# Kernel tuning notes

Measured on AMD Instinct MI355X. Metric: run time of the kernel, lower is better.

The kernel has to match this reference:

```python
import jax, jax.numpy as jnp
import numpy as np


def setup_inputs() -> dict:
    key = jax.random.key(0)
    k1, k2, k3 = jax.random.split(key, 3)
    S, B, H, D = 1024, 32, 512, 1024  # max_len, batch, bin_rnn_size, bin_rep_size
    hidden = jax.random.normal(k1, (2, B, H), dtype=jnp.float32)
    encoder_outputs = jax.random.normal(k2, (S, B, D), dtype=jnp.float32)
    # nn.Linear(D, D) params; scale W for numerically sane softmax logits
    W = jax.random.normal(k3, (D, D), dtype=jnp.float32) / np.float32(np.sqrt(D))
    b = jnp.zeros((D,), dtype=jnp.float32)
    return {"hidden": hidden, "encoder_outputs": encoder_outputs, "W": W, "b": b}


def reference(hidden, encoder_outputs, W, b):
    # method == 'general'
    B = hidden.shape[1]
    # torch.reshape((-1, B, 2H)).squeeze() == C-order flatten -> [B, 2H]
    h = hidden.reshape(B, -1)                                   # [B, D]
    energy = jnp.einsum('sbd,ed->sbe', encoder_outputs, W) + b  # Linear: x @ W.T + b
    # batch_product_luong + sum over features == contraction
    attn_energies = jnp.einsum('bd,sbd->bs', h, energy)         # [B, S]
    alpha = jax.nn.softmax(attn_energies, axis=1)[:, None, :]   # [B, 1, S]
    # alpha.bmm(encoder_outputs.transpose(0,1)) -> [B, 1, D]
    reps = jnp.einsum('bos,sbd->bod', alpha, encoder_outputs)
    return (reps, alpha)
```

## Files before the change

kernel.cpp:

```cpp
#include <hip/hip_runtime.h>

#define S 1024
#define B 32
#define D 1024
#define NCH 32
#define CH (S / NCH)
#define RPW (CH / 4)
#define NPAIR (RPW / 2)
#define ECH 8
#define EC 128

#define PG_OFF   0
#define LOG_OFF  (PG_OFF + ECH * B * D)
#define MARR_OFF (LOG_OFF + B * S)
#define LARR_OFF (MARR_OFF + NCH * B)
#define PACC_OFF (LARR_OFF + NCH * B)

__global__ __launch_bounds__(256) void kG(const float* __restrict__ hid,
                                          const float* __restrict__ W,
                                          float* __restrict__ ws) {
    const int d  = blockIdx.x * 256 + threadIdx.x;
    const int b  = blockIdx.y;
    const int e0 = blockIdx.z * EC;
    const float* __restrict__ hrow = hid + b * D;
    float acc = 0.f;
    #pragma unroll 8
    for (int e = e0; e < e0 + EC; ++e)
        acc = fmaf(hrow[e], W[(size_t)e * D + d], acc);
    ws[PG_OFF + ((size_t)blockIdx.z * B + b) * D + d] = acc;
}

__global__ __launch_bounds__(256) void kB(const float* __restrict__ enc,
                                          float* __restrict__ ws) {
    const int tid  = threadIdx.x;
    const int lane = tid & 63;
    const int wid  = tid >> 6;
    const int c    = blockIdx.x;
    const int b    = blockIdx.y;

    float* pg     = ws + PG_OFF;
    float* logits = ws + LOG_OFF;
    float* marr   = ws + MARR_OFF;
    float* larr   = ws + LARR_OFF;
    float* pacc   = ws + PACC_OFF;

    __shared__ float4 g_sh[256];
    __shared__ float4 sacc[4 * 256];
    __shared__ float sm[4], sl[4];

    const float4* encb = (const float4*)enc;
    const int row0 = c * CH + wid * RPW;
    const size_t rstride = (size_t)B * (D / 4);
    size_t base = ((size_t)row0 * B + b) * (D / 4) + lane;

    float4 cur[8], nxt[8];
    #pragma unroll
    for (int j = 0; j < 4; ++j) {
        cur[j]     = encb[base + j * 64];
        cur[4 + j] = encb[base + rstride + j * 64];
    }
    #pragma unroll
    for (int j = 0; j < 4; ++j) {
        nxt[j]     = encb[base + 2 * rstride + j * 64];
        nxt[4 + j] = encb[base + 3 * rstride + j * 64];
    }

    {
        float4 s4 = {0.f, 0.f, 0.f, 0.f};
        #pragma unroll
        for (int ec = 0; ec < ECH; ++ec) {
            float4 v = ((const float4*)(pg + (size_t)(ec * B + b) * D))[tid];
            s4.x += v.x; s4.y += v.y; s4.z += v.z; s4.w += v.w;
        }
        g_sh[tid] = s4;
    }
    __syncthreads();
    float4 gv[4];
    #pragma unroll
    for (int j = 0; j < 4; ++j) gv[j] = g_sh[j * 64 + lane];

    float m = -3.0e38f, l = 0.f;
    float4 acc[4] = {{0,0,0,0},{0,0,0,0},{0,0,0,0},{0,0,0,0}};

    #pragma unroll
    for (int p = 0; p < NPAIR; ++p) {
        float pd0 = 0.f, pd1 = 0.f;
        #pragma unroll
        for (int j = 0; j < 4; ++j) {
            pd0 += cur[j].x * gv[j].x + cur[j].y * gv[j].y +
                   cur[j].z * gv[j].z + cur[j].w * gv[j].w;
            pd1 += cur[4+j].x * gv[j].x + cur[4+j].y * gv[j].y +
                   cur[4+j].z * gv[j].z + cur[4+j].w * gv[j].w;
        }
        #pragma unroll
        for (int off = 1; off < 64; off <<= 1) {
            pd0 += __shfl_xor(pd0, off, 64);
            pd1 += __shfl_xor(pd1, off, 64);
        }
        if (lane == 0) {
            logits[b * S + row0 + 2 * p]     = pd0;
            logits[b * S + row0 + 2 * p + 1] = pd1;
        }
        float mn  = fmaxf(m, pd0);
        float sc0 = __expf(m - mn);
        float pA  = __expf(pd0 - mn);
        float mn2 = fmaxf(mn, pd1);
        float sc1 = __expf(mn - mn2);
        float pB  = __expf(pd1 - mn2);
        float s01 = sc0 * sc1;
        float a0  = pA * sc1;
        l = l * s01 + a0 + pB;
        #pragma unroll
        for (int j = 0; j < 4; ++j) {
            acc[j].x = acc[j].x * s01 + a0 * cur[j].x + pB * cur[4+j].x;
            acc[j].y = acc[j].y * s01 + a0 * cur[j].y + pB * cur[4+j].y;
            acc[j].z = acc[j].z * s01 + a0 * cur[j].z + pB * cur[4+j].z;
            acc[j].w = acc[j].w * s01 + a0 * cur[j].w + pB * cur[4+j].w;
        }
        m = mn2;
        if (p + 1 < NPAIR) {
            #pragma unroll
            for (int j = 0; j < 8; ++j) cur[j] = nxt[j];
        }
        if (p + 2 < NPAIR) {
            size_t nb = base + (size_t)(2 * (p + 2)) * rstride;
            #pragma unroll
            for (int j = 0; j < 4; ++j) {
                nxt[j]     = encb[nb + j * 64];
                nxt[4 + j] = encb[nb + rstride + j * 64];
            }
        }
    }

    #pragma unroll
    for (int j = 0; j < 4; ++j) sacc[wid * 256 + j * 64 + lane] = acc[j];
    if (lane == 0) { sm[wid] = m; sl[wid] = l; }
    __syncthreads();
    float mg = fmaxf(fmaxf(sm[0], sm[1]), fmaxf(sm[2], sm[3]));
    float4 r = {0.f, 0.f, 0.f, 0.f};
    float lsum = 0.f;
    #pragma unroll
    for (int w = 0; w < 4; ++w) {
        float fw = __expf(sm[w] - mg);
        float4 a = sacc[w * 256 + wid * 64 + lane];
        r.x += a.x * fw; r.y += a.y * fw; r.z += a.z * fw; r.w += a.w * fw;
        lsum += sl[w] * fw;
    }
    ((float4*)pacc)[(size_t)(c * B + b) * (D / 4) + tid] = r;
    if (tid == 0) { marr[c * B + b] = mg; larr[c * B + b] = lsum; }
}

__global__ __launch_bounds__(256) void kC(float* __restrict__ out,
                                          const float* __restrict__ ws) {
    const int tid = threadIdx.x;
    const int q   = blockIdx.x;
    const int b   = blockIdx.y;
    const float* logits = ws + LOG_OFF;
    const float* marr   = ws + MARR_OFF;
    const float* larr   = ws + LARR_OFF;
    const float* pacc   = ws + PACC_OFF;

    __shared__ float shm[NCH], shl[NCH], shf[NCH];
    if (tid < NCH) { shm[tid] = marr[tid * B + b]; shl[tid] = larr[tid * B + b]; }
    __syncthreads();
    float mg = -3.0e38f;
    #pragma unroll
    for (int cc = 0; cc < NCH; ++cc) mg = fmaxf(mg, shm[cc]);
    if (tid < NCH) shf[tid] = __expf(shm[tid] - mg);
    __syncthreads();
    float lg = 0.f;
    #pragma unroll
    for (int cc = 0; cc < NCH; ++cc) lg += shl[cc] * shf[cc];
    const float inv = 1.f / lg;

    if (tid < 64) {
        const int d4 = q * 64 + tid;
        float4 racc = {0.f, 0.f, 0.f, 0.f};
        #pragma unroll 4
        for (int cc = 0; cc < NCH; ++cc) {
            float  fc = shf[cc];
            float4 v  = ((const float4*)pacc)[(size_t)(cc * B + b) * (D / 4) + d4];
            racc.x += v.x * fc; racc.y += v.y * fc;
            racc.z += v.z * fc; racc.w += v.w * fc;
        }
        float4 rep = {racc.x * inv, racc.y * inv, racc.z * inv, racc.w * inv};
        ((float4*)out)[b * (D / 4) + d4] = rep;
    }
    const int s = q * 256 + tid;
    out[B * D + b * S + s] = __expf(logits[b * S + s] - mg) * inv;
}

extern "C" void kernel_launch(void* const* d_in, const int* in_sizes, int n_in,
                              void* d_out, int out_size, void* d_ws, size_t ws_size,
                              hipStream_t stream) {
    const float* hid = (const float*)d_in[0];
    const float* enc = (const float*)d_in[1];
    const float* W   = (const float*)d_in[2];

    float* out = (float*)d_out;
    float* ws  = (float*)d_ws;

    kG<<<dim3(D / 256, B, ECH), 256, 0, stream>>>(hid, W, ws);
    kB<<<dim3(NCH, B), 256, 0, stream>>>(enc, ws);
    kC<<<dim3(4, B), 256, 0, stream>>>(out, ws);
}
```

Before: 41.53 us.

## Stage encoder rows into LDS with async global_load_lds double buffering

Each block of the attention/softmax kernel now processes every row pair with all four waves, not one slice of rows per wave. Rows are streamed into a double-buffered shared-memory tile using the async global-to-LDS load builtin. Partial dot products are combined across waves through shared memory with a barrier per row pair. This removes the cross-wave online-softmax merge at the end and the register-file prefetch buffers. In exchange it has less memory traffic in flight and a block-wide barrier on every step, and it relies on the barrier to wait for the async LDS loads.

New measurement: 43.85 us. 1.06x slower.

```diff
diff --git a/kernel.cpp b/kernel.cpp
--- a/kernel.cpp
+++ b/kernel.cpp
@@ -1,12 +1,12 @@
 #include <hip/hip_runtime.h>
+#include <stdint.h>
 
 #define S 1024
 #define B 32
 #define D 1024
 #define NCH 32
 #define CH (S / NCH)
-#define RPW (CH / 4)
-#define NPAIR (RPW / 2)
+#define NPAIR (CH / 2)
 #define ECH 8
 #define EC 128
 
@@ -15,6 +15,9 @@
 #define MARR_OFF (LOG_OFF + B * S)
 #define LARR_OFF (MARR_OFF + NCH * B)
 #define PACC_OFF (LARR_OFF + NCH * B)
+
+typedef const __attribute__((address_space(1))) unsigned int* gas_t;
+typedef __attribute__((address_space(3))) unsigned int* las_t;
 
 __global__ __launch_bounds__(256) void kG(const float* __restrict__ hid,
                                           const float* __restrict__ W,
@@ -44,110 +47,78 @@
     float* larr   = ws + LARR_OFF;
     float* pacc   = ws + PACC_OFF;
 
-    __shared__ float4 g_sh[256];
-    __shared__ float4 sacc[4 * 256];
-    __shared__ float sm[4], sl[4];
+    __shared__ float tile[2][2 * D];
+    __shared__ float red[2][2][4];
 
-    const float4* encb = (const float4*)enc;
-    const int row0 = c * CH + wid * RPW;
-    const size_t rstride = (size_t)B * (D / 4);
-    size_t base = ((size_t)row0 * B + b) * (D / 4) + lane;
+    const int row0 = c * CH;
 
-    float4 cur[8], nxt[8];
+    auto stage = [&](int buf, int p) {
+        #pragma unroll
+        for (int r = 0; r < 2; ++r) {
+            const float* gp = enc + ((size_t)(row0 + 2 * p + r) * B + b) * D
+                            + wid * 256 + lane * 4;
+            float* lp = &tile[buf][r * D + wid * 256];
+            __builtin_amdgcn_global_load_lds((gas_t)(uintptr_t)gp,
+                                             (las_t)(uintptr_t)lp, 16, 0, 0);
+        }
+    };
+
+    stage(0, 0);
+
+    float4 gv = {0.f, 0.f, 0.f, 0.f};
     #pragma unroll
-    for (int j = 0; j < 4; ++j) {
-        cur[j]     = encb[base + j * 64];
-        cur[4 + j] = encb[base + rstride + j * 64];
-    }
-    #pragma unroll
-    for (int j = 0; j < 4; ++j) {
-        nxt[j]     = encb[base + 2 * rstride + j * 64];
-        nxt[4 + j] = encb[base + 3 * rstride + j * 64];
-    }
-
-    {
-        float4 s4 = {0.f, 0.f, 0.f, 0.f};
-        #pragma unroll
-        for (int ec = 0; ec < ECH; ++ec) {
-            float4 v = ((const float4*)(pg + (size_t)(ec * B + b) * D))[tid];
-            s4.x += v.x; s4.y += v.y; s4.z += v.z; s4.w += v.w;
-        }
-        g_sh[tid] = s4;
+    for (int ec = 0; ec < ECH; ++ec) {
+        float4 v = ((const float4*)(pg + (size_t)(ec * B + b) * D))[tid];
+        gv.x += v.x; gv.y += v.y; gv.z += v.z; gv.w += v.w;
     }
     __syncthreads();
-    float4 gv[4];
-    #pragma unroll
-    for (int j = 0; j < 4; ++j) gv[j] = g_sh[j * 64 + lane];
 
     float m = -3.0e38f, l = 0.f;
-    float4 acc[4] = {{0,0,0,0},{0,0,0,0},{0,0,0,0},{0,0,0,0}};
+    float4 acc = {0.f, 0.f, 0.f, 0.f};
 
-    #pragma unroll
     for (int p = 0; p < NPAIR; ++p) {
-        float pd0 = 0.f, pd1 = 0.f;
-        #pragma unroll
-        for (int j = 0; j < 4; ++j) {
-            pd0 += cur[j].x * gv[j].x + cur[j].y * gv[j].y +
-                   cur[j].z * gv[j].z + cur[j].w * gv[j].w;
-            pd1 += cur[4+j].x * gv[j].x + cur[4+j].y * gv[j].y +
-                   cur[4+j].z * gv[j].z + cur[4+j].w * gv[j].w;
-        }
+        const int cur = p & 1;
+        if (p + 1 < NPAIR) stage(cur ^ 1, p + 1);
+
+        const float4* t4 = (const float4*)tile[cur];
+        float4 e0 = t4[tid];
+        float4 e1 = t4[256 + tid];
+        float pd0 = e0.x * gv.x + e0.y * gv.y + e0.z * gv.z + e0.w * gv.w;
+        float pd1 = e1.x * gv.x + e1.y * gv.y + e1.z * gv.z + e1.w * gv.w;
         #pragma unroll
         for (int off = 1; off < 64; off <<= 1) {
             pd0 += __shfl_xor(pd0, off, 64);
             pd1 += __shfl_xor(pd1, off, 64);
         }
-        if (lane == 0) {
-            logits[b * S + row0 + 2 * p]     = pd0;
-            logits[b * S + row0 + 2 * p + 1] = pd1;
+        if (lane == 0) { red[p & 1][0][wid] = pd0; red[p & 1][1][wid] = pd1; }
+        __syncthreads();
+
+        float l0 = red[p & 1][0][0] + red[p & 1][0][1]
+                 + red[p & 1][0][2] + red[p & 1][0][3];
+        float l1 = red[p & 1][1][0] + red[p & 1][1][1]
+                 + red[p & 1][1][2] + red[p & 1][1][3];
+        if (tid == 0) {
+            logits[b * S + row0 + 2 * p]     = l0;
+            logits[b * S + row0 + 2 * p + 1] = l1;
         }
-        float mn  = fmaxf(m, pd0);
+        float mn  = fmaxf(m, l0);
         float sc0 = __expf(m - mn);
-        float pA  = __expf(pd0 - mn);
-        float mn2 = fmaxf(mn, pd1);
+        float pA  = __expf(l0 - mn);
+        float mn2 = fmaxf(mn, l1);
         float sc1 = __expf(mn - mn2);
-        float pB  = __expf(pd1 - mn2);
+        float pB  = __expf(l1 - mn2);
         float s01 = sc0 * sc1;
         float a0  = pA * sc1;
         l = l * s01 + a0 + pB;
-        #pragma unroll
-        for (int j = 0; j < 4; ++j) {
-            acc[j].x = acc[j].x * s01 + a0 * cur[j].x + pB * cur[4+j].x;
-            acc[j].y = acc[j].y * s01 + a0 * cur[j].y + pB * cur[4+j].y;
-            acc[j].z = acc[j].z * s01 + a0 * cur[j].z + pB * cur[4+j].z;
-            acc[j].w = acc[j].w * s01 + a0 * cur[j].w + pB * cur[4+j].w;
-        }
+        acc.x = acc.x * s01 + a0 * e0.x + pB * e1.x;
+        acc.y = acc.y * s01 + a0 * e0.y + pB * e1.y;
+        acc.z = acc.z * s01 + a0 * e0.z + pB * e1.z;
+        acc.w = acc.w * s01 + a0 * e0.w + pB * e1.w;
         m = mn2;
-        if (p + 1 < NPAIR) {
-            #pragma unroll
-            for (int j = 0; j < 8; ++j) cur[j] = nxt[j];
-        }
-        if (p + 2 < NPAIR) {
-            size_t nb = base + (size_t)(2 * (p + 2)) * rstride;
-            #pragma unroll
-            for (int j = 0; j < 4; ++j) {
-                nxt[j]     = encb[nb + j * 64];
-                nxt[4 + j] = encb[nb + rstride + j * 64];
-            }
-        }
     }
 
-    #pragma unroll
-    for (int j = 0; j < 4; ++j) sacc[wid * 256 + j * 64 + lane] = acc[j];
-    if (lane == 0) { sm[wid] = m; sl[wid] = l; }
-    __syncthreads();
-    float mg = fmaxf(fmaxf(sm[0], sm[1]), fmaxf(sm[2], sm[3]));
-    float4 r = {0.f, 0.f, 0.f, 0.f};
-    float lsum = 0.f;
-    #pragma unroll
-    for (int w = 0; w < 4; ++w) {
-        float fw = __expf(sm[w] - mg);
-        float4 a = sacc[w * 256 + wid * 64 + lane];
-        r.x += a.x * fw; r.y += a.y * fw; r.z += a.z * fw; r.w += a.w * fw;
-        lsum += sl[w] * fw;
-    }
-    ((float4*)pacc)[(size_t)(c * B + b) * (D / 4) + tid] = r;
-    if (tid == 0) { marr[c * B + b] = mg; larr[c * B + b] = lsum; }
+    ((float4*)pacc)[(size_t)(c * B + b) * (D / 4) + tid] = acc;
+    if (tid == 0) { marr[c * B + b] = m; larr[c * B + b] = l; }
 }
 
 __global__ __launch_bounds__(256) void kC(float* __restrict__ out,
```
